# Kernel tuning notes

Measured on AMD Instinct MI355X. Metric: run time of the kernel, lower is better.

Reference implementation:

```python
import jax, jax.numpy as jnp
import numpy as np

HOPS = 3  # max_hops; C has HOPS+1 tables

def setup_inputs() -> dict:
    key = jax.random.key(0)
    k1, k2, k3 = jax.random.split(key, 3)
    B, M, S, V, D = 32, 512, 10, 32000, 128
    story = jax.random.randint(k1, (B, M, S), 0, V)
    hidden = jax.random.normal(k2, (B, 1, D), dtype=jnp.float32)
    # hop+1 embedding tables, initialized N(0, 0.1) like the torch module
    C = 0.1 * jax.random.normal(k3, (HOPS + 1, V, D), dtype=jnp.float32)
    return {"story": story, "hidden": hidden, "C": C}

def reference(story, hidden, C):
    # story: [B, M, S] int tokens; hidden: [B, 1, D]; C: [HOPS+1, V, D]
    u = jnp.squeeze(hidden, axis=1)  # [B, D]
    prob_logit = None
    for h in range(HOPS):
        # embedding gather + bag-sum over sentence dim -> [B, M, D]
        embed_A = jnp.take(C[h], story, axis=0).sum(axis=2)
        # dot-product attention logits against current query u
        prob_logit = jnp.einsum('bmd,bd->bm', embed_A, u)  # [B, M]
        prob = jax.nn.softmax(prob_logit, axis=1)
        # second table gather + bag-sum, then softmax-weighted combine
        embed_C = jnp.take(C[h + 1], story, axis=0).sum(axis=2)  # [B, M, D]
        o_k = jnp.einsum('bm,bmd->bd', prob, embed_C)  # [B, D]
        u = u + o_k
    return prob_logit, u
```

## Files before the change

### kernel.cpp

```cpp
#include <hip/hip_runtime.h>

#define BB 32
#define MM 512
#define SS 10
#define VV 32000
#define DD 128
#define HOPS 3
#define BM (BB * MM)
#define NCHUNK 32
#define CHM (MM / NCHUNK)
#define PSTRIDE 132
#define UTP ((size_t)VV * 32)

__device__ __forceinline__ unsigned bfrn(float f) {
    unsigned u = __float_as_uint(f);
    return (u + 0x7FFFu + ((u >> 16) & 1u)) >> 16;
}
__device__ __forceinline__ unsigned pk(float a, float b) { return bfrn(a) | (bfrn(b) << 16); }
__device__ __forceinline__ float bflo(unsigned q) { return __uint_as_float(q << 16); }
__device__ __forceinline__ float bfhi(unsigned q) { return __uint_as_float(q & 0xFFFF0000u); }

__device__ __forceinline__ void cvt_pair_unit(const float* __restrict__ CA,
                                              const float* __restrict__ CB,
                                              unsigned* __restrict__ dst, size_t g) {
    const size_t v = g >> 5, j = g & 31;
    const float4 a = ((const float4*)CA)[v * 32 + j];
    const float4 b = ((const float4*)CB)[v * 32 + j];
    uint4 o;
    o.x = pk(a.x, a.y);
    o.y = pk(b.x, b.y);
    o.z = pk(a.z, a.w);
    o.w = pk(b.z, b.w);
    ((uint4*)dst)[v * 32 + j] = o;
}


__global__ __launch_bounds__(256) void cvt01(const float* __restrict__ Cmat,
                                             unsigned* __restrict__ Cb01) {
    const size_t g = (size_t)blockIdx.x * 256 + threadIdx.x;
    if (g < UTP)
        cvt_pair_unit(Cmat, Cmat + (size_t)VV * DD, Cb01, g);
}

__device__ __forceinline__ void write_partial(const int b, const int c,
                                              const int w, const int lane,
                                              float nx, float ny, float den,
                                              float* __restrict__ pout,
                                              float (*sx)[64], float (*sy)[64],
                                              float* sd) {
    sx[w][lane] = nx; sy[w][lane] = ny;
    if (lane == 0) sd[w] = den;
    __syncthreads();
    if (w == 0) {
        const float ox = sx[0][lane] + sx[1][lane] + sx[2][lane] + sx[3][lane];
        const float oy = sy[0][lane] + sy[1][lane] + sy[2][lane] + sy[3][lane];
        float* prow = pout + ((size_t)b * NCHUNK + c) * PSTRIDE;
        ((float2*)prow)[lane] = make_float2(ox, oy);
        if (lane == 0) prow[DD] = sd[0] + sd[1] + sd[2] + sd[3];
    }
}

__global__ __launch_bounds__(256) void hop0_k(const int* __restrict__ story,
                                              const unsigned* __restrict__ Cb01,
                                              const float* __restrict__ hidden,
                                              unsigned* __restrict__ E1,
                                              float* __restrict__ P0,
                                              const float* __restrict__ Cmat,
                                              unsigned* __restrict__ Cb23) {
    const int b = blockIdx.y, c = blockIdx.x;
    const int tid = threadIdx.x;
    const int w = tid >> 6, lane = tid & 63;
    __shared__ float su[DD];
    __shared__ float sx[4][64], sy[4][64];
    __shared__ float sd[4];

    if (tid < DD) su[tid] = hidden[b * DD + tid];
    __syncthreads();
    const float2 uv = ((const float2*)su)[lane];
    const uint2* G = (const uint2*)Cb01;

    float nx = 0.f, ny = 0.f, den = 0.f;
#pragma unroll
    for (int k = 0; k < CHM / 4; ++k) {
        const int m = c * CHM + k * 4 + w;
        const int bm = b * MM + m;
        int tok[SS];
        const int* st = story + (size_t)bm * SS;
#pragma unroll
        for (int s = 0; s < SS; ++s) tok[s] = st[s];

        float ex = 0.f, ey = 0.f, rx = 0.f, ry = 0.f;
#pragma unroll
        for (int s = 0; s < SS; ++s) {
            const uint2 q = G[(size_t)tok[s] * 64 + lane];
            ex += bflo(q.x); ey += bfhi(q.x);
            rx += bflo(q.y); ry += bfhi(q.y);
        }
        float l = ex * uv.x + ey * uv.y;
#pragma unroll
        for (int off = 32; off; off >>= 1) l += __shfl_xor(l, off, 64);
        const float e = expf(l);

        E1[(size_t)bm * 64 + lane] = pk(rx, ry);
        nx += e * rx; ny += e * ry; den += e;
    }
    write_partial(b, c, w, lane, nx, ny, den, P0, sx, sy, sd);

    const size_t t0 = (((size_t)blockIdx.y * gridDim.x + blockIdx.x) * 256 + tid) * 4;
#pragma unroll
    for (int i = 0; i < 4; ++i) {
        const size_t g = t0 + i;
        if (g < UTP)
            cvt_pair_unit(Cmat + (size_t)2 * VV * DD, Cmat + (size_t)3 * VV * DD,
                          Cb23, g);
    }
}

__global__ __launch_bounds__(256) void hop1_k(const int* __restrict__ story,
                                              const unsigned* __restrict__ Cb23,
                                              const unsigned* __restrict__ E1,
                                              const float* __restrict__ hidden,
                                              const float* __restrict__ P0,
                                              float* __restrict__ u1,
                                              unsigned* __restrict__ E23,
                                              float* __restrict__ P1) {
    const int b = blockIdx.y, c = blockIdx.x;
    const int tid = threadIdx.x;
    const int w = tid >> 6, lane = tid & 63;
    __shared__ float su[DD];
    __shared__ float sx[4][64], sy[4][64];
    __shared__ float sd[4];

    if (tid < DD) {
        float num = 0.f, dsum = 0.f;
        for (int cc = 0; cc < NCHUNK; ++cc) {
            const float* p = P0 + ((size_t)b * NCHUNK + cc) * PSTRIDE;
            num += p[tid];
            dsum += p[DD];
        }
        const float v = hidden[b * DD + tid] + num / dsum;
        if (c == 0) u1[b * DD + tid] = v;
        su[tid] = v;
    }
    __syncthreads();
    const float2 uv = ((const float2*)su)[lane];

    float nx = 0.f, ny = 0.f, den = 0.f;
#pragma unroll
    for (int k = 0; k < CHM / 4; ++k) {
        const int m = c * CHM + k * 4 + w;
        const int bm = b * MM + m;
        int tok[SS];
        const int* st = story + (size_t)bm * SS;
#pragma unroll
        for (int s = 0; s < SS; ++s) tok[s] = st[s];

        const unsigned eq = E1[(size_t)bm * 64 + lane];
        float l = bflo(eq) * uv.x + bfhi(eq) * uv.y;
#pragma unroll
        for (int off = 32; off; off >>= 1) l += __shfl_xor(l, off, 64);
        const float e = expf(l);

        float r2x = 0.f, r2y = 0.f, r3x = 0.f, r3y = 0.f;
#pragma unroll
        for (int s = 0; s < SS; ++s) {
            const uint2 q = ((const uint2*)Cb23)[(size_t)tok[s] * 64 + lane];
            r2x += bflo(q.x); r2y += bfhi(q.x);
            r3x += bflo(q.y); r3y += bfhi(q.y);
        }
        ((uint2*)E23)[(size_t)bm * 64 + lane] = make_uint2(pk(r2x, r2y), pk(r3x, r3y));
        nx += e * r2x; ny += e * r2y; den += e;
    }
    write_partial(b, c, w, lane, nx, ny, den, P1, sx, sy, sd);
}

__global__ __launch_bounds__(1024) void hop2_final(const unsigned* __restrict__ E23,
                                                   const float* __restrict__ u1,
                                                   const float* __restrict__ P1,
                                                   float* __restrict__ logit,
                                                   float* __restrict__ uout) {
    const int b = blockIdx.x;
    const int tid = threadIdx.x;
    const int w = tid >> 6, lane = tid & 63;
    __shared__ float su[DD];
    __shared__ float sx[16][64], sy[16][64];
    __shared__ float sd[16];

    if (tid < DD) {
        float num = 0.f, dsum = 0.f;
        for (int cc = 0; cc < NCHUNK; ++cc) {
            const float* p = P1 + ((size_t)b * NCHUNK + cc) * PSTRIDE;
            num += p[tid];
            dsum += p[DD];
        }
        su[tid] = u1[b * DD + tid] + num / dsum;
    }
    __syncthreads();
    const float2 uv = ((const float2*)su)[lane];

    float nx = 0.f, ny = 0.f, den = 0.f;
#pragma unroll 4
    for (int m = w * 32; m < w * 32 + 32; ++m) {
        const int bm = b * MM + m;
        const uint2 q = ((const uint2*)E23)[(size_t)bm * 64 + lane];
        float l = bflo(q.x) * uv.x + bfhi(q.x) * uv.y;
#pragma unroll
        for (int off = 32; off; off >>= 1) l += __shfl_xor(l, off, 64);
        if (lane == 0) logit[bm] = l;
        const float e = expf(l);
        nx += e * bflo(q.y); ny += e * bfhi(q.y); den += e;
    }

    sx[w][lane] = nx; sy[w][lane] = ny;
    if (lane == 0) sd[w] = den;
    __syncthreads();
    if (w == 0) {
        float ox = 0.f, oy = 0.f, od = 0.f;
#pragma unroll
        for (int i = 0; i < 16; ++i) { ox += sx[i][lane]; oy += sy[i][lane]; od += sd[i]; }
        const float2 u2 = ((const float2*)su)[lane];
        ((float2*)(uout + b * DD))[lane] = make_float2(u2.x + ox / od, u2.y + oy / od);
    }
}

__global__ __launch_bounds__(256) void init_u(const float* __restrict__ hidden,
                                              float* __restrict__ u) {
    int i = blockIdx.x * 256 + threadIdx.x;
    if (i < BB * DD) u[i] = hidden[i];
}

__global__ __launch_bounds__(256) void logit_kernel(const int* __restrict__ story,
                                                    const float* __restrict__ Ch,
                                                    const float* __restrict__ u,
                                                    float* __restrict__ logit) {
    int wid = (blockIdx.x * 256 + threadIdx.x) >> 6;
    int lane = threadIdx.x & 63;
    if (wid >= BB * MM) return;
    int b = wid >> 9;
    const int* st = story + (size_t)wid * SS;
    int tok[SS];
#pragma unroll
    for (int s = 0; s < SS; ++s) tok[s] = st[s];
    float ax = 0.f, ay = 0.f;
#pragma unroll
    for (int s = 0; s < SS; ++s) {
        const float2 v = ((const float2*)(Ch + (size_t)tok[s] * DD))[lane];
        ax += v.x; ay += v.y;
    }
    const float2 uv = ((const float2*)(u + b * DD))[lane];
    float p = ax * uv.x + ay * uv.y;
#pragma unroll
    for (int off = 32; off; off >>= 1) p += __shfl_down(p, off, 64);
    if (lane == 0) logit[wid] = p;
}

__global__ __launch_bounds__(256) void softmax_kernel(const float* __restrict__ logit,
                                                      float* __restrict__ prob) {
    int b = blockIdx.x;
    int t = threadIdx.x;
    __shared__ float red[8];
    float l0 = logit[b * MM + t];
    float l1 = logit[b * MM + 256 + t];
    float mx = fmaxf(l0, l1);
#pragma unroll
    for (int off = 32; off; off >>= 1) mx = fmaxf(mx, __shfl_xor(mx, off, 64));
    if ((t & 63) == 0) red[t >> 6] = mx;
    __syncthreads();
    mx = fmaxf(fmaxf(red[0], red[1]), fmaxf(red[2], red[3]));
    float e0 = expf(l0 - mx), e1 = expf(l1 - mx);
    float s = e0 + e1;
#pragma unroll
    for (int off = 32; off; off >>= 1) s += __shfl_xor(s, off, 64);
    if ((t & 63) == 0) red[4 + (t >> 6)] = s;
    __syncthreads();
    s = red[4] + red[5] + red[6] + red[7];
    float inv = 1.0f / s;
    prob[b * MM + t] = e0 * inv;
    prob[b * MM + 256 + t] = e1 * inv;
}

__global__ __launch_bounds__(256) void partial_kernel(const int* __restrict__ story,
                                                      const float* __restrict__ Ch1,
                                                      const float* __restrict__ prob,
                                                      float* __restrict__ partial,
                                                      int chunk) {
    int b = blockIdx.y, c = blockIdx.x;
    int w = threadIdx.x >> 6, lane = threadIdx.x & 63;
    int m0 = c * chunk;
    float ax = 0.f, ay = 0.f;
    for (int m = m0 + w; m < m0 + chunk; m += 4) {
        float pw = prob[b * MM + m];
        const int* st = story + (size_t)(b * MM + m) * SS;
        int tok[SS];
#pragma unroll
        for (int s = 0; s < SS; ++s) tok[s] = st[s];
        float sx = 0.f, sy = 0.f;
#pragma unroll
        for (int s = 0; s < SS; ++s) {
            const float2 v = ((const float2*)(Ch1 + (size_t)tok[s] * DD))[lane];
            sx += v.x; sy += v.y;
        }
        ax += pw * sx; ay += pw * sy;
    }
    __shared__ float redx[4][64];
    __shared__ float redy[4][64];
    redx[w][lane] = ax;
    redy[w][lane] = ay;
    __syncthreads();
    if (w == 0) {
        float ox = redx[0][lane] + redx[1][lane] + redx[2][lane] + redx[3][lane];
        float oy = redy[0][lane] + redy[1][lane] + redy[2][lane] + redy[3][lane];
        float2* dst = (float2*)(partial + ((size_t)b * gridDim.x + c) * DD);
        dst[lane] = make_float2(ox, oy);
    }
}

__global__ __launch_bounds__(256) void update_kernel(const float* __restrict__ partial,
                                                     float* __restrict__ u, int NC) {
    int i = blockIdx.x * 256 + threadIdx.x;
    if (i >= BB * DD) return;
    int b = i >> 7, d = i & 127;
    float s = 0.f;
    for (int c = 0; c < NC; ++c) s += partial[((size_t)b * NC + c) * DD + d];
    u[i] += s;
}

extern "C" void kernel_launch(void* const* d_in, const int* in_sizes, int n_in,
                              void* d_out, int out_size, void* d_ws, size_t ws_size,
                              hipStream_t stream) {
    const int*   story  = (const int*)d_in[0];
    const float* hidden = (const float*)d_in[1];
    const float* Cmat   = (const float*)d_in[2];

    float* out   = (float*)d_out;
    float* logit = out;
    float* uout  = out + BB * MM;

    const size_t szCbp = (size_t)VV * 128;
    const size_t szE1  = (size_t)BM * 64;
    const size_t szE23 = (size_t)BM * 128;
    const size_t szP   = (size_t)BB * NCHUNK * PSTRIDE;
    const size_t need  = (2 * szCbp + szE1 + szE23 + 2 * szP + BB * DD) * sizeof(float);

    if (ws_size >= need) {
        unsigned* Cb01 = (unsigned*)d_ws;
        unsigned* Cb23 = Cb01 + szCbp;
        unsigned* E1   = Cb23 + szCbp;
        unsigned* E23  = E1 + szE1;
        float*    P0   = (float*)(E23 + szE23);
        float*    P1   = P0 + szP;
        float*    u1   = P1 + szP;

        cvt01<<<(unsigned)((UTP + 255) / 256), 256, 0, stream>>>(Cmat, Cb01);
        hop0_k<<<dim3(NCHUNK, BB), 256, 0, stream>>>(story, Cb01, hidden, E1, P0,
                                                     Cmat, Cb23);
        hop1_k<<<dim3(NCHUNK, BB), 256, 0, stream>>>(story, Cb23, E1, hidden,
                                                     P0, u1, E23, P1);
        hop2_final<<<BB, 1024, 0, stream>>>(E23, u1, P1, logit, uout);
    } else {
        float* prob = (float*)d_ws;
        int NC = 32;
        while (NC > 1 && (size_t)(BB * MM + BB * NC * DD) * 4 > ws_size) NC >>= 1;
        float* partial = prob + BB * MM;
        int chunk = MM / NC;

        init_u<<<(BB * DD + 255) / 256, 256, 0, stream>>>(hidden, uout);
        for (int h = 0; h < HOPS; ++h) {
            const float* Ca = Cmat + (size_t)h * VV * DD;
            const float* Cc = Cmat + (size_t)(h + 1) * VV * DD;
            logit_kernel<<<(BB * MM) / 4, 256, 0, stream>>>(story, Ca, uout, logit);
            softmax_kernel<<<BB, 256, 0, stream>>>(logit, prob);
            partial_kernel<<<dim3(NC, BB), 256, 0, stream>>>(story, Cc, prob, partial, chunk);
            update_kernel<<<(BB * DD + 255) / 256, 256, 0, stream>>>(partial, uout, NC);
        }
    }
}
```

Baseline: 72.33 us.

## Split final hop across chunked blocks and add small reduction kernel

The last hop previously ran on only 32 blocks of 1024 threads, one per batch. It now runs on a grid of 32 chunks by 32 batches, each block writing partial softmax numerators and denominators. A new tiny kernel then combines those partials into the output query. This raises parallelism across the GPU's compute units at the cost of one extra launch and an extra partial buffer round-trip.

```diff
diff --git a/kernel.cpp b/kernel.cpp
--- a/kernel.cpp
+++ b/kernel.cpp
@@ -174,17 +174,18 @@
     write_partial(b, c, w, lane, nx, ny, den, P1, sx, sy, sd);
 }
 
-__global__ __launch_bounds__(1024) void hop2_final(const unsigned* __restrict__ E23,
-                                                   const float* __restrict__ u1,
-                                                   const float* __restrict__ P1,
-                                                   float* __restrict__ logit,
-                                                   float* __restrict__ uout) {
-    const int b = blockIdx.x;
+__global__ __launch_bounds__(256) void hop2_k(const unsigned* __restrict__ E23,
+                                              const float* __restrict__ u1,
+                                              const float* __restrict__ P1,
+                                              float* __restrict__ u2,
+                                              float* __restrict__ logit,
+                                              float* __restrict__ P2) {
+    const int b = blockIdx.y, c = blockIdx.x;
     const int tid = threadIdx.x;
     const int w = tid >> 6, lane = tid & 63;
     __shared__ float su[DD];
-    __shared__ float sx[16][64], sy[16][64];
-    __shared__ float sd[16];
+    __shared__ float sx[4][64], sy[4][64];
+    __shared__ float sd[4];
 
     if (tid < DD) {
         float num = 0.f, dsum = 0.f;
@@ -193,14 +194,17 @@
             num += p[tid];
             dsum += p[DD];
         }
-        su[tid] = u1[b * DD + tid] + num / dsum;
+        const float v = u1[b * DD + tid] + num / dsum;
+        if (c == 0) u2[b * DD + tid] = v;
+        su[tid] = v;
     }
     __syncthreads();
     const float2 uv = ((const float2*)su)[lane];
 
     float nx = 0.f, ny = 0.f, den = 0.f;
-#pragma unroll 4
-    for (int m = w * 32; m < w * 32 + 32; ++m) {
+#pragma unroll
+    for (int k = 0; k < CHM / 4; ++k) {
+        const int m = c * CHM + k * 4 + w;
         const int bm = b * MM + m;
         const uint2 q = ((const uint2*)E23)[(size_t)bm * 64 + lane];
         float l = bflo(q.x) * uv.x + bfhi(q.x) * uv.y;
@@ -210,17 +214,20 @@
         const float e = expf(l);
         nx += e * bflo(q.y); ny += e * bfhi(q.y); den += e;
     }
-
-    sx[w][lane] = nx; sy[w][lane] = ny;
-    if (lane == 0) sd[w] = den;
-    __syncthreads();
-    if (w == 0) {
-        float ox = 0.f, oy = 0.f, od = 0.f;
-#pragma unroll
-        for (int i = 0; i < 16; ++i) { ox += sx[i][lane]; oy += sy[i][lane]; od += sd[i]; }
-        const float2 u2 = ((const float2*)su)[lane];
-        ((float2*)(uout + b * DD))[lane] = make_float2(u2.x + ox / od, u2.y + oy / od);
-    }
+    write_partial(b, c, w, lane, nx, ny, den, P2, sx, sy, sd);
+}
+
+__global__ __launch_bounds__(128) void final_u(const float* __restrict__ pin,
+                                               const float* __restrict__ u2,
+                                               float* __restrict__ uout) {
+    const int b = blockIdx.x, d = threadIdx.x;
+    float num = 0.f, den = 0.f;
+    for (int cc = 0; cc < NCHUNK; ++cc) {
+        const float* p = pin + ((size_t)b * NCHUNK + cc) * PSTRIDE;
+        num += p[d];
+        den += p[DD];
+    }
+    uout[b * DD + d] = u2[b * DD + d] + num / den;
 }
 
 __global__ __launch_bounds__(256) void init_u(const float* __restrict__ hidden,
@@ -340,7 +347,8 @@
     const size_t szE1  = (size_t)BM * 64;
     const size_t szE23 = (size_t)BM * 128;
     const size_t szP   = (size_t)BB * NCHUNK * PSTRIDE;
-    const size_t need  = (2 * szCbp + szE1 + szE23 + 2 * szP + BB * DD) * sizeof(float);
+    const size_t need  = (2 * szCbp + szE1 + szE23 + 3 * szP + 2 * BB * DD)
+                         * sizeof(float);
 
     if (ws_size >= need) {
         unsigned* Cb01 = (unsigned*)d_ws;
@@ -349,14 +357,17 @@
         unsigned* E23  = E1 + szE1;
         float*    P0   = (float*)(E23 + szE23);
         float*    P1   = P0 + szP;
-        float*    u1   = P1 + szP;
+        float*    P2   = P1 + szP;
+        float*    u1   = P2 + szP;
+        float*    u2   = u1 + BB * DD;
 
         cvt01<<<(unsigned)((UTP + 255) / 256), 256, 0, stream>>>(Cmat, Cb01);
         hop0_k<<<dim3(NCHUNK, BB), 256, 0, stream>>>(story, Cb01, hidden, E1, P0,
                                                      Cmat, Cb23);
         hop1_k<<<dim3(NCHUNK, BB), 256, 0, stream>>>(story, Cb23, E1, hidden,
                                                      P0, u1, E23, P1);
-        hop2_final<<<BB, 1024, 0, stream>>>(E23, u1, P1, logit, uout);
+        hop2_k<<<dim3(NCHUNK, BB), 256, 0, stream>>>(E23, u1, P1, u2, logit, P2);
+        final_u<<<BB, 128, 0, stream>>>(P2, u2, uout);
     } else {
         float* prob = (float*)d_ws;
         int NC = 32;
```

Measured after the change: 63.81 us. -11.8%, faster.
